# Performance work log

Measured on AMD Instinct MI355X. Metric: run time of the kernel, lower is better.

## Reference

```python
import jax, jax.numpy as jnp
import numpy as np
from jax.ops import segment_sum

N = 102400          # num nodes
E = 1638400         # num edges (avg degree 16)
F_IN = 128          # node_feature_dim
H = 128             # hidden_dim
L = 2               # num_layers
B = 64              # num graphs
NPG = N // B        # nodes per graph (equal-size graphs -> static dense shape)


def setup_inputs() -> dict:
    key = jax.random.key(0)
    ks = jax.random.split(key, 8)
    x = jax.random.normal(ks[0], (N, F_IN), dtype=jnp.float32)
    edge_index = jax.random.randint(ks[1], (2, E), 0, N, dtype=jnp.int64)
    batch = (jnp.arange(N, dtype=jnp.int64) // NPG)  # sorted, equal-size graphs
    s_in = 1.0 / np.sqrt(F_IN)
    s_h = 1.0 / np.sqrt(H)
    W_in = jax.random.uniform(ks[2], (F_IN, H), jnp.float32, -s_in, s_in)
    b_in = jax.random.uniform(ks[3], (H,), jnp.float32, -s_in, s_in)
    Ws = jax.random.uniform(ks[4], (L, H, H), jnp.float32, -s_h, s_h)
    bs = jax.random.uniform(ks[5], (L, H), jnp.float32, -s_h, s_h)
    return {"x": x, "edge_index": edge_index, "batch": batch,
            "W_in": W_in, "b_in": b_in, "Ws": Ws, "bs": bs}


def _gcn_conv(x, W, b, src, dst):
    # PyG GCNConv: self-loops + symmetric deg^-1/2 normalization + scatter-add
    h = x @ W                                            # [N, H]
    loops = jnp.arange(N, dtype=src.dtype)
    s = jnp.concatenate([src, loops])                    # [E+N]
    d = jnp.concatenate([dst, loops])
    deg = segment_sum(jnp.ones_like(d, dtype=h.dtype), d, num_segments=N)
    dinv = jnp.where(deg > 0, jax.lax.rsqrt(deg), 0.0)   # deg^-0.5, inf->0
    norm = dinv[s] * dinv[d]                             # [E+N]
    msg = h[s] * norm[:, None]                           # gather + scale
    out = segment_sum(msg, d, num_segments=N)            # scatter-add at target
    return out + b


def reference(x, edge_index, batch, W_in, b_in, Ws, bs):
    src, dst = edge_index[0], edge_index[1]
    h = x @ W_in + b_in                                  # node_feature_transform
    for l in range(L):
        h = jax.nn.relu(_gcn_conv(h, Ws[l], bs[l], src, dst))
        # dropout(0.1) is identity in eval mode
    # to_dense_batch: batch is sorted with exactly NPG nodes per graph
    dense = h.reshape(B, NPG, H)                          # [B, max_nodes, H]
    return dense
```

## Files before the change

kernel.cpp:

```cpp
#include <hip/hip_runtime.h>
#include <hip/hip_bf16.h>

#define NNODES 102400
#define NEDGES 1638400
#define HD 128
#define ZROW_OFF (NNODES * 256)

typedef float f32x4 __attribute__((ext_vector_type(4)));
typedef short short8 __attribute__((ext_vector_type(8)));
typedef unsigned short ushort8 __attribute__((ext_vector_type(8)));
typedef unsigned int uint32;

static __device__ __forceinline__ unsigned short f2bf(float v) {
  union { float f; unsigned u; } x; x.f = v;
  unsigned r = x.u + 0x7fffu + ((x.u >> 16) & 1u);
  return (unsigned short)(r >> 16);
}
static __device__ __forceinline__ float bflo(uint32 u) { return __uint_as_float(u << 16); }
static __device__ __forceinline__ float bfhi(uint32 u) { return __uint_as_float(u & 0xffff0000u); }

__global__ __launch_bounds__(256) void k_deg(const int* __restrict__ dst, int* __restrict__ cnt,
                                             int* __restrict__ rank) {
  int e = blockIdx.x * 256 + threadIdx.x;
  rank[e] = atomicAdd(&cnt[dst[e]], 1);
}

__global__ __launch_bounds__(256) void k_scan1(const int* __restrict__ cnt, int* __restrict__ rowptr,
                                               int* __restrict__ partials, float* __restrict__ dinv) {
  __shared__ int s[256];
  int t = threadIdx.x;
  int i = blockIdx.x * 256 + t;
  int v = cnt[i];
  dinv[i] = rsqrtf((float)v + 1.0f);
  int vp = (v + 3) & ~3;
  s[t] = vp; __syncthreads();
  for (int off = 1; off < 256; off <<= 1) {
    int x = (t >= off) ? s[t - off] : 0;
    __syncthreads();
    s[t] += x; __syncthreads();
  }
  rowptr[i] = s[t] - vp;
  if (t == 255) partials[blockIdx.x] = s[t];
}

__global__ __launch_bounds__(512) void k_scan2(int* __restrict__ partials) {
  __shared__ int s[512];
  int t = threadIdx.x;
  int v = (t < 400) ? partials[t] : 0;
  s[t] = v; __syncthreads();
  for (int off = 1; off < 512; off <<= 1) {
    int x = (t >= off) ? s[t - off] : 0;
    __syncthreads();
    s[t] += x; __syncthreads();
  }
  if (t < 400) partials[t] = s[t] - v;
}

__global__ __launch_bounds__(256) void k_scan3(int* __restrict__ rowptr, const int* __restrict__ partials,
                                               const int* __restrict__ cnt, int* __restrict__ csr) {
  int i = blockIdx.x * 256 + threadIdx.x;
  int base = rowptr[i] + partials[blockIdx.x];
  rowptr[i] = base;
  int v = cnt[i];
  int vp = (v + 3) & ~3;
  for (int t = v; t < vp; ++t) csr[base + t] = ZROW_OFF;
  if (i == NNODES - 1) rowptr[NNODES] = base + vp;
}

__global__ __launch_bounds__(256) void k_fill(const int* __restrict__ src, const int* __restrict__ dst,
                                              const int* __restrict__ rank, const int* __restrict__ rowptr,
                                              int* __restrict__ csr) {
  int e = blockIdx.x * 256 + threadIdx.x;
  int s = src[e], d = dst[e];
  csr[rowptr[d] + rank[e]] = s * 256;
}

__global__ __launch_bounds__(256) void k_prep(const float* __restrict__ W_in, const float* __restrict__ Ws,
                                              const float* __restrict__ b_in,
                                              unsigned short* __restrict__ WT0, unsigned short* __restrict__ WT1,
                                              float* __restrict__ bc) {
  int blk = blockIdx.x, tid = threadIdx.x;
  if (blk < 64) {
    int t = blk * 256 + tid;
    int c = t >> 7, k = t & 127;
    float acc = 0.f;
    #pragma unroll 4
    for (int j = 0; j < 128; ++j) acc += W_in[k * 128 + j] * Ws[j * 128 + c];
    WT0[c * 128 + k] = f2bf(acc);
  } else if (blk == 64) {
    if (tid < 128) {
      float acc = 0.f;
      #pragma unroll 4
      for (int j = 0; j < 128; ++j) acc += b_in[j] * Ws[j * 128 + tid];
      bc[tid] = acc;
    }
  } else {
    int t = (blk - 65) * 256 + tid;
    int c = t >> 7, k = t & 127;
    WT1[c * 128 + k] = f2bf(Ws[128 * 128 + k * 128 + c]);
  }
}

template<bool IN_F32, bool ADD_BIAS, bool SCALE>
__global__ __launch_bounds__(256) void k_gemm(const void* __restrict__ inp, const unsigned short* __restrict__ WT,
                                              const float* __restrict__ bias, const float* __restrict__ dinv,
                                              unsigned short* __restrict__ outp) {
  __shared__ unsigned short sA[128][136];
  __shared__ unsigned short sB[128][136];
  const int tid = threadIdx.x;
  const size_t r0 = (size_t)blockIdx.x * 128;

  #pragma unroll
  for (int i = 0; i < 8; ++i) {
    int f = tid + i * 256;
    int c = f >> 4, u = f & 15;
    *(ushort8*)&sB[c][u * 8] = *(const ushort8*)&WT[(size_t)c * 128 + u * 8];
  }
  if constexpr (IN_F32) {
    const float* in = (const float*)inp;
    #pragma unroll
    for (int i = 0; i < 8; ++i) {
      int f = tid + i * 256;
      int row = f >> 4, u = f & 15;
      const float4 v0 = *(const float4*)&in[(r0 + row) * 128 + u * 8];
      const float4 v1 = *(const float4*)&in[(r0 + row) * 128 + u * 8 + 4];
      ushort8 pk;
      pk[0] = f2bf(v0.x); pk[1] = f2bf(v0.y); pk[2] = f2bf(v0.z); pk[3] = f2bf(v0.w);
      pk[4] = f2bf(v1.x); pk[5] = f2bf(v1.y); pk[6] = f2bf(v1.z); pk[7] = f2bf(v1.w);
      *(ushort8*)&sA[row][u * 8] = pk;
    }
  } else {
    const unsigned short* in = (const unsigned short*)inp;
    #pragma unroll
    for (int i = 0; i < 8; ++i) {
      int f = tid + i * 256;
      int row = f >> 4, u = f & 15;
      *(ushort8*)&sA[row][u * 8] = *(const ushort8*)&in[(r0 + row) * 128 + u * 8];
    }
  }
  __syncthreads();

  const int lane = tid & 63;
  const int wv = tid >> 6;
  const int wr = wv >> 1, wc = wv & 1;
  const int lrow = lane & 15, lg = lane >> 4;

  f32x4 acc[4][4];
  #pragma unroll
  for (int m = 0; m < 4; ++m)
    #pragma unroll
    for (int n = 0; n < 4; ++n)
      acc[m][n] = (f32x4){0.f, 0.f, 0.f, 0.f};

  #pragma unroll
  for (int kt = 0; kt < 4; ++kt) {
    short8 a[4], b[4];
    #pragma unroll
    for (int m = 0; m < 4; ++m)
      a[m] = *(const short8*)&sA[wr * 64 + m * 16 + lrow][kt * 32 + lg * 8];
    #pragma unroll
    for (int n = 0; n < 4; ++n)
      b[n] = *(const short8*)&sB[wc * 64 + n * 16 + lrow][kt * 32 + lg * 8];
    #pragma unroll
    for (int m = 0; m < 4; ++m)
      #pragma unroll
      for (int n = 0; n < 4; ++n)
        acc[m][n] = __builtin_amdgcn_mfma_f32_16x16x32_bf16(a[m], b[n], acc[m][n], 0, 0, 0);
  }

  #pragma unroll
  for (int m = 0; m < 4; ++m) {
    size_t row0 = r0 + wr * 64 + m * 16 + lg * 4;
    float4 dv = {1.f, 1.f, 1.f, 1.f};
    if constexpr (SCALE) dv = *(const float4*)&dinv[row0];
    #pragma unroll
    for (int n = 0; n < 4; ++n) {
      int col = wc * 64 + n * 16 + lrow;
      float bv = ADD_BIAS ? bias[col] : 0.0f;
      f32x4 v = acc[m][n];
      #pragma unroll
      for (int r = 0; r < 4; ++r) {
        float o = v[r] + bv;
        if constexpr (SCALE) o *= ((const float*)&dv)[r];
        outp[(row0 + r) * 128 + col] = f2bf(o);
      }
    }
  }
}

template<bool OUT_F32>
__global__ __launch_bounds__(256) void k_agg(const unsigned short* __restrict__ g, const int* __restrict__ csr,
                                             const int* __restrict__ rowptr, const float* __restrict__ dinv,
                                             const float* __restrict__ bias, void* __restrict__ outp) {
  int n = blockIdx.x * 4 + (threadIdx.x >> 6);
  int lane = threadIdx.x & 63;
  const char* gb = (const char*)g;
  const int lo4 = lane * 4;

  uint32 sv = *(const uint32*)(gb + (size_t)(n * 256 + lo4));
  float accx = bflo(sv), accy = bfhi(sv);
  int j = rowptr[n], je = rowptr[n + 1];

#define LD(off) (*(const uint32*)(gb + (size_t)(unsigned)((off) + lo4)))
  for (; j + 16 <= je; j += 16) {
    int4 c0 = *(const int4*)&csr[j];
    int4 c1 = *(const int4*)&csr[j + 4];
    int4 c2 = *(const int4*)&csr[j + 8];
    int4 c3 = *(const int4*)&csr[j + 12];
    uint32 q0 = LD(c0.x), q1 = LD(c0.y), q2 = LD(c0.z), q3 = LD(c0.w);
    uint32 q4 = LD(c1.x), q5 = LD(c1.y), q6 = LD(c1.z), q7 = LD(c1.w);
    uint32 q8 = LD(c2.x), q9 = LD(c2.y), qa = LD(c2.z), qb = LD(c2.w);
    uint32 qc = LD(c3.x), qd = LD(c3.y), qe = LD(c3.z), qf = LD(c3.w);
    accx += bflo(q0) + bflo(q1) + bflo(q2) + bflo(q3)
          + bflo(q4) + bflo(q5) + bflo(q6) + bflo(q7)
          + bflo(q8) + bflo(q9) + bflo(qa) + bflo(qb)
          + bflo(qc) + bflo(qd) + bflo(qe) + bflo(qf);
    accy += bfhi(q0) + bfhi(q1) + bfhi(q2) + bfhi(q3)
          + bfhi(q4) + bfhi(q5) + bfhi(q6) + bfhi(q7)
          + bfhi(q8) + bfhi(q9) + bfhi(qa) + bfhi(qb)
          + bfhi(qc) + bfhi(qd) + bfhi(qe) + bfhi(qf);
  }
  if (j + 8 <= je) {
    int4 c0 = *(const int4*)&csr[j];
    int4 c1 = *(const int4*)&csr[j + 4];
    uint32 q0 = LD(c0.x), q1 = LD(c0.y), q2 = LD(c0.z), q3 = LD(c0.w);
    uint32 q4 = LD(c1.x), q5 = LD(c1.y), q6 = LD(c1.z), q7 = LD(c1.w);
    accx += bflo(q0) + bflo(q1) + bflo(q2) + bflo(q3)
          + bflo(q4) + bflo(q5) + bflo(q6) + bflo(q7);
    accy += bfhi(q0) + bfhi(q1) + bfhi(q2) + bfhi(q3)
          + bfhi(q4) + bfhi(q5) + bfhi(q6) + bfhi(q7);
    j += 8;
  }
  if (j + 4 <= je) {
    int4 c0 = *(const int4*)&csr[j];
    uint32 q0 = LD(c0.x), q1 = LD(c0.y), q2 = LD(c0.z), q3 = LD(c0.w);
    accx += bflo(q0) + bflo(q1) + bflo(q2) + bflo(q3);
    accy += bfhi(q0) + bfhi(q1) + bfhi(q2) + bfhi(q3);
  }
#undef LD

  float dn = dinv[n];
  float2 b2 = ((const float2*)bias)[lane];
  accx = fmaxf(fmaf(accx, dn, b2.x), 0.0f);
  accy = fmaxf(fmaf(accy, dn, b2.y), 0.0f);
  if constexpr (OUT_F32) {
    ((float2*)outp)[(size_t)n * 64 + lane] = make_float2(accx, accy);
  } else {
    uint32 pk = ((uint32)f2bf(accy) << 16) | (uint32)f2bf(accx);
    ((uint32*)outp)[(size_t)n * 64 + lane] = pk;
  }
}

extern "C" void kernel_launch(void* const* d_in, const int* in_sizes, int n_in,
                              void* d_out, int out_size, void* d_ws, size_t ws_size,
                              hipStream_t stream) {
  const float* x    = (const float*)d_in[0];
  const int*   ei   = (const int*)d_in[1];
  const float* W_in = (const float*)d_in[3];
  const float* b_in = (const float*)d_in[4];
  const float* Ws   = (const float*)d_in[5];
  const float* bs   = (const float*)d_in[6];
  float* out = (float*)d_out;
  const int* src = ei;
  const int* dst = ei + NEDGES;

  char* ws = (char*)d_ws;
  size_t off = 0;
  auto alloc = [&](size_t bytes) { void* p = ws + off; off = (off + bytes + 255) & ~(size_t)255; return p; };
  unsigned short* Bb  = (unsigned short*)alloc((size_t)NNODES * 128 * 2 + 512);
  unsigned short* A   = (unsigned short*)alloc((size_t)NNODES * 128 * 2);
  unsigned short* WT0 = (unsigned short*)alloc((size_t)128 * 128 * 2);
  unsigned short* WT1 = (unsigned short*)alloc((size_t)128 * 128 * 2);
  float* bc      = (float*)alloc(128 * 4);
  int*   cnt     = (int*)alloc((size_t)NNODES * 4);
  int*   rowptr  = (int*)alloc((size_t)(NNODES + 1) * 4);
  int*   partials= (int*)alloc(512 * 4);
  float* dinv    = (float*)alloc((size_t)NNODES * 4);
  int*   csr     = (int*)alloc((size_t)(NEDGES + 3 * NNODES) * 4);
  int*   rank    = (int*)A;

  hipMemsetAsync(cnt, 0, (size_t)NNODES * 4, stream);
  hipMemsetAsync(Bb + (size_t)NNODES * 128, 0, 512, stream);
  k_deg  <<<NEDGES / 256, 256, 0, stream>>>(dst, cnt, rank);
  k_scan1<<<NNODES / 256, 256, 0, stream>>>(cnt, rowptr, partials, dinv);
  k_scan2<<<1, 512, 0, stream>>>(partials);
  k_scan3<<<NNODES / 256, 256, 0, stream>>>(rowptr, partials, cnt, csr);
  k_fill <<<NEDGES / 256, 256, 0, stream>>>(src, dst, rank, rowptr, csr);
  k_prep <<<129, 256, 0, stream>>>(W_in, Ws, b_in, WT0, WT1, bc);

  k_gemm<true, true, true><<<NNODES / 128, 256, 0, stream>>>(x, WT0, bc, dinv, Bb);
  k_agg<false><<<NNODES / 4, 256, 0, stream>>>(Bb, csr, rowptr, dinv, bs, A);
  k_gemm<false, false, true><<<NNODES / 128, 256, 0, stream>>>(A, WT1, nullptr, dinv, Bb);
  k_agg<true><<<NNODES / 4, 256, 0, stream>>>(Bb, csr, rowptr, dinv, bs + 128, out);
}
```

Measured before the change: 363.7 us.

## Replace global atomic degree counting with per-block sliced LDS histograms

The global atomicAdd degree count and per-edge rank kernel is replaced by a histogram kernel. Each of 128 blocks counts its edge chunk's destinations in shared-memory slices and writes per-block 16-bit counts and local ranks. The scan kernel then builds per-block offsets for each node with an exclusive scan down the block axis, and CSR fill combines rowptr, block offset and local rank. This aims to remove contended global atomics. In exchange it writes and re-reads a large per-block count matrix (about 26 MB, stored in the Bb buffer), runs only 128 blocks, and makes an extra random gather in the fill kernel.

```diff
diff --git a/kernel.cpp b/kernel.cpp
--- a/kernel.cpp
+++ b/kernel.cpp
@@ -6,6 +6,13 @@
 #define HD 128
 #define ZROW_OFF (NNODES * 256)
 
+#define NB 128
+#define NT 512
+#define EPB (NEDGES / NB)
+#define EIT (EPB / NT)
+#define NSLICE 8
+#define SLICE (NNODES / NSLICE)
+
 typedef float f32x4 __attribute__((ext_vector_type(4)));
 typedef short short8 __attribute__((ext_vector_type(8)));
 typedef unsigned short ushort8 __attribute__((ext_vector_type(8)));
@@ -19,20 +26,52 @@
 static __device__ __forceinline__ float bflo(uint32 u) { return __uint_as_float(u << 16); }
 static __device__ __forceinline__ float bfhi(uint32 u) { return __uint_as_float(u & 0xffff0000u); }
 
-__global__ __launch_bounds__(256) void k_deg(const int* __restrict__ dst, int* __restrict__ cnt,
-                                             int* __restrict__ rank) {
-  int e = blockIdx.x * 256 + threadIdx.x;
-  rank[e] = atomicAdd(&cnt[dst[e]], 1);
-}
-
-__global__ __launch_bounds__(256) void k_scan1(const int* __restrict__ cnt, int* __restrict__ rowptr,
-                                               int* __restrict__ partials, float* __restrict__ dinv) {
+__global__ __launch_bounds__(NT) void k_hist(const int* __restrict__ dst,
+                                             unsigned short* __restrict__ blkcnt,
+                                             unsigned short* __restrict__ lrank16) {
+  __shared__ int hist[SLICE];
+  const int blk = blockIdx.x, tid = threadIdx.x;
+  const int e0 = blk * EPB;
+  int dreg[EIT];
+  #pragma unroll
+  for (int i = 0; i < EIT; ++i) dreg[i] = dst[e0 + i * NT + tid];
+
+  for (int p = 0; p < NSLICE; ++p) {
+    const int lo = p * SLICE;
+    for (int i = tid; i < SLICE; i += NT) hist[i] = 0;
+    __syncthreads();
+    #pragma unroll
+    for (int i = 0; i < EIT; ++i) {
+      int r = dreg[i] - lo;
+      if ((unsigned)r < (unsigned)SLICE) {
+        int lr = atomicAdd(&hist[r], 1);
+        lrank16[e0 + i * NT + tid] = (unsigned short)lr;
+      }
+    }
+    __syncthreads();
+    for (int i = tid; i < SLICE; i += NT)
+      blkcnt[(size_t)blk * NNODES + lo + i] = (unsigned short)hist[i];
+    __syncthreads();
+  }
+}
+
+__global__ __launch_bounds__(256) void k_scan1(unsigned short* __restrict__ blkcnt,
+                                               int* __restrict__ rowptr, int* __restrict__ partials,
+                                               float* __restrict__ dinv, int* __restrict__ degs) {
   __shared__ int s[256];
   int t = threadIdx.x;
   int i = blockIdx.x * 256 + t;
-  int v = cnt[i];
-  dinv[i] = rsqrtf((float)v + 1.0f);
-  int vp = (v + 3) & ~3;
+  int run = 0;
+  #pragma unroll 8
+  for (int b = 0; b < NB; ++b) {
+    size_t idx = (size_t)b * NNODES + i;
+    int c = blkcnt[idx];
+    blkcnt[idx] = (unsigned short)run;
+    run += c;
+  }
+  degs[i] = run;
+  dinv[i] = rsqrtf((float)run + 1.0f);
+  int vp = (run + 3) & ~3;
   s[t] = vp; __syncthreads();
   for (int off = 1; off < 256; off <<= 1) {
     int x = (t >= off) ? s[t - off] : 0;
@@ -57,22 +96,26 @@
 }
 
 __global__ __launch_bounds__(256) void k_scan3(int* __restrict__ rowptr, const int* __restrict__ partials,
-                                               const int* __restrict__ cnt, int* __restrict__ csr) {
+                                               const int* __restrict__ degs, int* __restrict__ csr) {
   int i = blockIdx.x * 256 + threadIdx.x;
   int base = rowptr[i] + partials[blockIdx.x];
   rowptr[i] = base;
-  int v = cnt[i];
+  int v = degs[i];
   int vp = (v + 3) & ~3;
   for (int t = v; t < vp; ++t) csr[base + t] = ZROW_OFF;
   if (i == NNODES - 1) rowptr[NNODES] = base + vp;
 }
 
 __global__ __launch_bounds__(256) void k_fill(const int* __restrict__ src, const int* __restrict__ dst,
-                                              const int* __restrict__ rank, const int* __restrict__ rowptr,
+                                              const unsigned short* __restrict__ lrank16,
+                                              const int* __restrict__ rowptr,
+                                              const unsigned short* __restrict__ blkcnt,
                                               int* __restrict__ csr) {
   int e = blockIdx.x * 256 + threadIdx.x;
   int s = src[e], d = dst[e];
-  csr[rowptr[d] + rank[e]] = s * 256;
+  int b = e / EPB;
+  int slot = rowptr[d] + (int)blkcnt[(size_t)b * NNODES + d] + (int)lrank16[e];
+  csr[slot] = s * 256;
 }
 
 __global__ __launch_bounds__(256) void k_prep(const float* __restrict__ W_in, const float* __restrict__ Ws,
@@ -272,20 +315,20 @@
   unsigned short* WT0 = (unsigned short*)alloc((size_t)128 * 128 * 2);
   unsigned short* WT1 = (unsigned short*)alloc((size_t)128 * 128 * 2);
   float* bc      = (float*)alloc(128 * 4);
-  int*   cnt     = (int*)alloc((size_t)NNODES * 4);
   int*   rowptr  = (int*)alloc((size_t)(NNODES + 1) * 4);
   int*   partials= (int*)alloc(512 * 4);
   float* dinv    = (float*)alloc((size_t)NNODES * 4);
+  int*   degs    = (int*)alloc((size_t)NNODES * 4);
   int*   csr     = (int*)alloc((size_t)(NEDGES + 3 * NNODES) * 4);
-  int*   rank    = (int*)A;
-
-  hipMemsetAsync(cnt, 0, (size_t)NNODES * 4, stream);
+  unsigned short* blkcnt  = (unsigned short*)Bb;
+  unsigned short* lrank16 = (unsigned short*)A;
+
   hipMemsetAsync(Bb + (size_t)NNODES * 128, 0, 512, stream);
-  k_deg  <<<NEDGES / 256, 256, 0, stream>>>(dst, cnt, rank);
-  k_scan1<<<NNODES / 256, 256, 0, stream>>>(cnt, rowptr, partials, dinv);
+  k_hist <<<NB, NT, 0, stream>>>(dst, blkcnt, lrank16);
+  k_scan1<<<NNODES / 256, 256, 0, stream>>>(blkcnt, rowptr, partials, dinv, degs);
   k_scan2<<<1, 512, 0, stream>>>(partials);
-  k_scan3<<<NNODES / 256, 256, 0, stream>>>(rowptr, partials, cnt, csr);
-  k_fill <<<NEDGES / 256, 256, 0, stream>>>(src, dst, rank, rowptr, csr);
+  k_scan3<<<NNODES / 256, 256, 0, stream>>>(rowptr, partials, degs, csr);
+  k_fill <<<NEDGES / 256, 256, 0, stream>>>(src, dst, lrank16, rowptr, blkcnt, csr);
   k_prep <<<129, 256, 0, stream>>>(W_in, Ws, b_in, WT0, WT1, bc);
 
   k_gemm<true, true, true><<<NNODES / 128, 256, 0, stream>>>(x, WT0, bc, dinv, Bb);
```

Measured after the change: 347.3 us. 1.05x faster.
